# Performance work log

Hardware: AMD Instinct MI355X
Metric: run time of the kernel (lower is better)

## Reference

```python
import jax, jax.numpy as jnp
import numpy as np

VOCAB = 400001  # vocab_size + 1
H = 100         # n_hidden
B = 512
T = 25
FC = 128
NC = 2
FORGET_BIAS = 1.0


def setup_inputs() -> dict:
    key = jax.random.key(0)
    ks = jax.random.split(key, 8)
    features = jax.random.randint(ks[0], (B, T), 0, VOCAB, dtype=jnp.int32)
    embedding = jax.random.normal(ks[1], (VOCAB, H), dtype=jnp.float32) * 0.05
    # BasicLSTMCell kernel: [input_dim + hidden, 4*hidden], gate order (i, j, f, o)
    k1 = jax.random.normal(ks[2], (2 * H, 4 * H), dtype=jnp.float32) * 0.05
    b1 = jnp.zeros((4 * H,), dtype=jnp.float32)
    k2 = jax.random.normal(ks[3], (2 * H, 4 * H), dtype=jnp.float32) * 0.05
    b2 = jnp.zeros((4 * H,), dtype=jnp.float32)
    w_fc1 = jax.random.normal(ks[4], (H, FC), dtype=jnp.float32) * 0.05
    b_fc1 = jnp.zeros((FC,), dtype=jnp.float32)
    w_fc2 = jax.random.normal(ks[5], (FC, NC), dtype=jnp.float32) * 0.05
    b_fc2 = jnp.zeros((NC,), dtype=jnp.float32)
    return {"features": features, "embedding": embedding,
            "k1": k1, "b1": b1, "k2": k2, "b2": b2,
            "w_fc1": w_fc1, "b_fc1": b_fc1, "w_fc2": w_fc2, "b_fc2": b_fc2}


def _lstm_cell(c, h, x, kernel, bias):
    z = jnp.concatenate([x, h], axis=-1) @ kernel + bias  # [B, 4H]
    i, j, f, o = jnp.split(z, 4, axis=-1)
    c_new = c * jax.nn.sigmoid(f + FORGET_BIAS) + jax.nn.sigmoid(i) * jnp.tanh(j)
    h_new = jnp.tanh(c_new) * jax.nn.sigmoid(o)
    return c_new, h_new


def reference(features, embedding, k1, b1, k2, b2, w_fc1, b_fc1, w_fc2, b_fc2):
    x = embedding[features]                      # [B, T, H]
    xs = jnp.swapaxes(x, 0, 1)                   # [T, B, H] for scan over time
    batch = features.shape[0]
    zeros = jnp.zeros((batch, H), dtype=embedding.dtype)

    def step(carry, xt):
        c1, h1, c2, h2 = carry
        c1, h1 = _lstm_cell(c1, h1, xt, k1, b1)
        c2, h2 = _lstm_cell(c2, h2, h1, k2, b2)
        return (c1, h1, c2, h2), None

    (c1, h1, c2, h2), _ = jax.lax.scan(step, (zeros, zeros, zeros, zeros), xs)
    # dynamic_rnn outputs[:, -1, :] == final top-layer hidden state h2
    fc1 = h2 @ w_fc1 + b_fc1                     # linear, no activation (tf.layers.dense default)
    pred = fc1 @ w_fc2 + b_fc2                   # [B, num_classes] logits
    return pred
```

## Files before the change

### kernel.cpp

```cpp
#include <hip/hip_runtime.h>
#include <cstdint>
#include <cstddef>

#define VOCABSZ 400001
#define Hn 100
#define Tn 25
#define Bn 512
#define FCn 128
#define Rr 2
#define NBLK (Bn / Rr)
#define NTHR 512

typedef _Float16 half2_t __attribute__((ext_vector_type(2)));

__device__ __forceinline__ half2_t h2bits(unsigned v) {
    union { unsigned u; half2_t h; } x; x.u = v; return x.h;
}
__device__ __forceinline__ float fdot2f(half2_t a, half2_t b, float c) {
    return __builtin_amdgcn_fdot2(a, b, c, false);
}
__device__ __forceinline__ float sigm(float x) {
    return __fdividef(1.0f, 1.0f + __expf(-x));
}
__device__ __forceinline__ float tanh_fast(float x) {
    float e = __expf(2.0f * x);
    return __fdividef(e - 1.0f, e + 1.0f);
}

__global__ void prep_weights(const float* __restrict__ k1,
                             const float* __restrict__ k2,
                             uint4* __restrict__ WP) {
    int t = blockIdx.x * blockDim.x + threadIdx.x;
    if (t >= 2 * 25 * 400) return;
    int l   = t / 10000;
    int rem = t % 10000;
    int kq  = rem / 400;
    int o   = rem % 400;
    int u = o >> 2, g = o & 3;
    int c = g * 100 + u;
    const float* K = l ? k2 : k1;
    union { unsigned u32; half2_t h; } d[4];
    #pragma unroll
    for (int j = 0; j < 4; j++) {
        int k0 = 8 * kq + 2 * j;
        d[j].h.x = (_Float16)K[(k0    ) * 400 + c];
        d[j].h.y = (_Float16)K[(k0 + 1) * 400 + c];
    }
    uint4 v; v.x = d[0].u32; v.y = d[1].u32; v.z = d[2].u32; v.w = d[3].u32;
    WP[t] = v;
}

__device__ __forceinline__ float lstm_update(float z, int g, float& cst) {
    float t1 = __shfl_xor(z, 1);
    float t2 = __shfl_xor(z, 2);
    float t3 = __shfl_xor(t1, 2);
    bool g0 = (g & 1) != 0, g1 = (g & 2) != 0;
    float vi = g1 ? (g0 ? t3 : t2) : (g0 ? t1 : z);
    float vj = g1 ? (g0 ? t2 : t3) : (g0 ? z  : t1);
    float vf = g1 ? (g0 ? t1 : z ) : (g0 ? t3 : t2);
    float vo = g1 ? (g0 ? z  : t1) : (g0 ? t2 : t3);
    cst = cst * sigm(vf + 1.0f) + sigm(vi) * tanh_fast(vj);
    return tanh_fast(cst) * sigm(vo);
}

#define GEMV_LAYER(SRC0, SRC1, LIDX, BIAS, Z0, Z1)                           \
  {                                                                          \
    const uint4* _p0 = (const uint4*)(SRC0);                                 \
    const uint4* _p1 = (const uint4*)(SRC1);                                 \
    uint4 _vx = _p0[lane < 25 ? lane : 0];                                   \
    uint4 _vy = _p1[lane < 25 ? lane : 0];                                   \
    float _a0=0.f,_a1=0.f,_a2=0.f,_a3=0.f;                                   \
    float _d0=0.f,_d1=0.f,_d2=0.f,_d3=0.f;                                   \
    _Pragma("unroll")                                                        \
    for (int kq = 0; kq < 25; kq++) {                                        \
      uint4 _w = w[LIDX][kq];                                                \
      unsigned _s0 = (unsigned)__builtin_amdgcn_readlane((int)_vx.x, kq);    \
      unsigned _s1 = (unsigned)__builtin_amdgcn_readlane((int)_vx.y, kq);    \
      unsigned _s2 = (unsigned)__builtin_amdgcn_readlane((int)_vx.z, kq);    \
      unsigned _s3 = (unsigned)__builtin_amdgcn_readlane((int)_vx.w, kq);    \
      _a0 = fdot2f(h2bits(_w.x), h2bits(_s0), _a0);                          \
      _a1 = fdot2f(h2bits(_w.y), h2bits(_s1), _a1);                          \
      _a2 = fdot2f(h2bits(_w.z), h2bits(_s2), _a2);                          \
      _a3 = fdot2f(h2bits(_w.w), h2bits(_s3), _a3);                          \
      unsigned _t0 = (unsigned)__builtin_amdgcn_readlane((int)_vy.x, kq);    \
      unsigned _t1 = (unsigned)__builtin_amdgcn_readlane((int)_vy.y, kq);    \
      unsigned _t2 = (unsigned)__builtin_amdgcn_readlane((int)_vy.z, kq);    \
      unsigned _t3 = (unsigned)__builtin_amdgcn_readlane((int)_vy.w, kq);    \
      _d0 = fdot2f(h2bits(_w.x), h2bits(_t0), _d0);                          \
      _d1 = fdot2f(h2bits(_w.y), h2bits(_t1), _d1);                          \
      _d2 = fdot2f(h2bits(_w.z), h2bits(_t2), _d2);                          \
      _d3 = fdot2f(h2bits(_w.w), h2bits(_t3), _d3);                          \
    }                                                                        \
    Z0 = _a0 + _a1 + _a2 + _a3 + (BIAS);                                     \
    Z1 = _d0 + _d1 + _d2 + _d3 + (BIAS);                                     \
  }

__global__ __launch_bounds__(NTHR, 2) void lstm_main(
    const int*   __restrict__ features,
    const float* __restrict__ embedding,
    const float* __restrict__ b1,
    const float* __restrict__ b2,
    const float* __restrict__ w_fc1,
    const float* __restrict__ b_fc1,
    const float* __restrict__ w_fc2,
    const float* __restrict__ b_fc2,
    const uint4* __restrict__ WP,
    float*       __restrict__ out)
{
    __shared__ _Float16 xh1[Rr][200];
    __shared__ _Float16 xh2[Rr][200];
    __shared__ float    wred[8][2];

    const int tid  = threadIdx.x;
    const int lane = tid & 63;
    const int o    = (tid < 400) ? tid : 399;
    const int u = o >> 2, g = o & 3;
    const int c = g * 100 + u;
    const bool owner = (tid < 400);

    uint4 w[2][25];
    #pragma unroll
    for (int l = 0; l < 2; l++)
        #pragma unroll
        for (int kq = 0; kq < 25; kq++)
            w[l][kq] = WP[(l * 25 + kq) * 400 + o];

    const float bias1 = b1[c];
    const float bias2 = b2[c];

    if (tid < 200) {
        int r = tid / 100, uu = tid % 100;
        xh1[r][100 + uu] = (_Float16)0.0f;
        xh2[r][uu]       = (_Float16)0.0f;
        xh2[r][100 + uu] = (_Float16)0.0f;
    }
    if (tid < 100) {
        int r = tid / 50, p = tid % 50;
        int f0 = features[(blockIdx.x * Rr + r) * Tn + 0];
        float2 e = *(const float2*)(embedding + (size_t)f0 * Hn + 2 * p);
        half2_t h; h.x = (_Float16)e.x; h.y = (_Float16)e.y;
        ((half2_t*)&xh1[r][0])[p] = h;
    }
    __syncthreads();

    float c1[Rr] = {0.f, 0.f}, c2[Rr] = {0.f, 0.f};
    float h1v[Rr] = {0.f, 0.f}, h2v[Rr] = {0.f, 0.f};

    for (int step = 0; step < Tn; step++) {
        float2 epre = {0.f, 0.f};
        int prow = 0, pp = 0;
        if (tid < 448) {
            if (owner && g == 1 && step + 1 < Tn) {
                prow = (u >= 50);
                pp   = u % 50;
                int f1 = features[(blockIdx.x * Rr + prow) * Tn + step + 1];
                epre = *(const float2*)(embedding + (size_t)f1 * Hn + 2 * pp);
            }
            float z0, z1;
            GEMV_LAYER(&xh1[0][0], &xh1[1][0], 0, bias1, z0, z1);
            h1v[0] = lstm_update(z0, g, c1[0]);
            h1v[1] = lstm_update(z1, g, c1[1]);
        }
        __syncthreads();
        if (owner) {
            if (g == 0) {
                xh1[0][100 + u] = (_Float16)h1v[0];
                xh1[1][100 + u] = (_Float16)h1v[1];
                xh2[0][u]       = (_Float16)h1v[0];
                xh2[1][u]       = (_Float16)h1v[1];
            }
            if (g == 1 && step + 1 < Tn) {
                half2_t h; h.x = (_Float16)epre.x; h.y = (_Float16)epre.y;
                ((half2_t*)&xh1[prow][0])[pp] = h;
            }
        }
        __syncthreads();
        if (tid < 448) {
            float z0, z1;
            GEMV_LAYER(&xh2[0][0], &xh2[1][0], 1, bias2, z0, z1);
            h2v[0] = lstm_update(z0, g, c2[0]);
            h2v[1] = lstm_update(z1, g, c2[1]);
        }
        __syncthreads();
        if (owner && g == 0) {
            xh2[0][100 + u] = (_Float16)h2v[0];
            xh2[1][100 + u] = (_Float16)h2v[1];
        }
    }
    __syncthreads();

    if (tid < Rr * FCn) {
        int r = tid >> 7;
        int j = tid & 127;
        float acc = b_fc1[j];
        #pragma unroll 10
        for (int uu = 0; uu < Hn; uu++)
            acc = fmaf((float)xh2[r][100 + uu], w_fc1[uu * FCn + j], acc);
        float p0 = acc * w_fc2[2 * j + 0];
        float p1 = acc * w_fc2[2 * j + 1];
        #pragma unroll
        for (int off = 32; off > 0; off >>= 1) {
            p0 += __shfl_down(p0, off, 64);
            p1 += __shfl_down(p1, off, 64);
        }
        if (lane == 0) {
            int wv = tid >> 6;
            wred[wv][0] = p0;
            wred[wv][1] = p1;
        }
    }
    __syncthreads();
    if (tid < 4) {
        int r = tid >> 1, cls = tid & 1;
        out[(blockIdx.x * Rr + r) * 2 + cls] =
            wred[2 * r][cls] + wred[2 * r + 1][cls] + b_fc2[cls];
    }
}

extern "C" void kernel_launch(void* const* d_in, const int* in_sizes, int n_in,
                              void* d_out, int out_size, void* d_ws, size_t ws_size,
                              hipStream_t stream) {
    const int*   features  = (const int*)  d_in[0];
    const float* embedding = (const float*)d_in[1];
    const float* k1        = (const float*)d_in[2];
    const float* b1        = (const float*)d_in[3];
    const float* k2        = (const float*)d_in[4];
    const float* b2        = (const float*)d_in[5];
    const float* w_fc1     = (const float*)d_in[6];
    const float* b_fc1     = (const float*)d_in[7];
    const float* w_fc2     = (const float*)d_in[8];
    const float* b_fc2     = (const float*)d_in[9];

    uint4* WP = (uint4*)d_ws;

    prep_weights<<<(20000 + 255) / 256, 256, 0, stream>>>(k1, k2, WP);
    lstm_main<<<NBLK, NTHR, 0, stream>>>(features, embedding, b1, b2,
                                         w_fc1, b_fc1, w_fc2, b_fc2,
                                         WP, (float*)d_out);
}
```

Baseline: 344.1 us.

## Stage layer-1 LSTM weights in LDS and tile the weight-prep transpose

The main kernel previously kept both layers' packed fp16 weights in registers (50 uint4 per thread). That register pressure likely caused spills under the launch bounds. Now the layer-1 weights (about 160 KB) are copied once into LDS per block and read from there each step, while only the layer-2 weights stay in registers. This adds per-step LDS read traffic and a large up-front LDS fill, and uses almost the whole LDS, limiting the CU to one block. The prep kernel also now stages an 8x400 slab through shared memory so the global reads are coalesced.

```diff
diff --git a/kernel.cpp b/kernel.cpp
--- a/kernel.cpp
+++ b/kernel.cpp
@@ -27,27 +27,31 @@
     return __fdividef(e - 1.0f, e + 1.0f);
 }
 
-__global__ void prep_weights(const float* __restrict__ k1,
-                             const float* __restrict__ k2,
-                             uint4* __restrict__ WP) {
-    int t = blockIdx.x * blockDim.x + threadIdx.x;
-    if (t >= 2 * 25 * 400) return;
-    int l   = t / 10000;
-    int rem = t % 10000;
-    int kq  = rem / 400;
-    int o   = rem % 400;
-    int u = o >> 2, g = o & 3;
-    int c = g * 100 + u;
+__global__ __launch_bounds__(512) void prep_weights(const float* __restrict__ k1,
+                                                    const float* __restrict__ k2,
+                                                    uint4* __restrict__ WP) {
+    __shared__ float tile[8][400];
+    int l  = blockIdx.x / 25;
+    int kq = blockIdx.x % 25;
     const float* K = l ? k2 : k1;
-    union { unsigned u32; half2_t h; } d[4];
-    #pragma unroll
-    for (int j = 0; j < 4; j++) {
-        int k0 = 8 * kq + 2 * j;
-        d[j].h.x = (_Float16)K[(k0    ) * 400 + c];
-        d[j].h.y = (_Float16)K[(k0 + 1) * 400 + c];
-    }
-    uint4 v; v.x = d[0].u32; v.y = d[1].u32; v.z = d[2].u32; v.w = d[3].u32;
-    WP[t] = v;
+    for (int i = threadIdx.x; i < 8 * 400; i += 512) {
+        int row = i / 400, col = i % 400;
+        tile[row][col] = K[(8 * kq + row) * 400 + col];
+    }
+    __syncthreads();
+    int o = threadIdx.x;
+    if (o < 400) {
+        int u = o >> 2, g = o & 3;
+        int c = g * 100 + u;
+        union { unsigned u32; half2_t h; } d[4];
+        #pragma unroll
+        for (int j = 0; j < 4; j++) {
+            d[j].h.x = (_Float16)tile[2 * j][c];
+            d[j].h.y = (_Float16)tile[2 * j + 1][c];
+        }
+        uint4 v; v.x = d[0].u32; v.y = d[1].u32; v.z = d[2].u32; v.w = d[3].u32;
+        WP[(l * 25 + kq) * 400 + o] = v;
+    }
 }
 
 __device__ __forceinline__ float lstm_update(float z, int g, float& cst) {
@@ -63,7 +67,7 @@
     return tanh_fast(cst) * sigm(vo);
 }
 
-#define GEMV_LAYER(SRC0, SRC1, LIDX, BIAS, Z0, Z1)                           \
+#define GEMV_W(WGET, SRC0, SRC1, BIAS, Z0, Z1)                               \
   {                                                                          \
     const uint4* _p0 = (const uint4*)(SRC0);                                 \
     const uint4* _p1 = (const uint4*)(SRC1);                                 \
@@ -73,7 +77,7 @@
     float _d0=0.f,_d1=0.f,_d2=0.f,_d3=0.f;                                   \
     _Pragma("unroll")                                                        \
     for (int kq = 0; kq < 25; kq++) {                                        \
-      uint4 _w = w[LIDX][kq];                                                \
+      uint4 _w = (WGET);                                                     \
       unsigned _s0 = (unsigned)__builtin_amdgcn_readlane((int)_vx.x, kq);    \
       unsigned _s1 = (unsigned)__builtin_amdgcn_readlane((int)_vx.y, kq);    \
       unsigned _s2 = (unsigned)__builtin_amdgcn_readlane((int)_vx.z, kq);    \
@@ -107,8 +111,9 @@
     const uint4* __restrict__ WP,
     float*       __restrict__ out)
 {
-    __shared__ _Float16 xh1[Rr][200];
-    __shared__ _Float16 xh2[Rr][200];
+    __shared__ uint4    ldsK1[10000];
+    __shared__ alignas(16) _Float16 xh1[Rr][200];
+    __shared__ alignas(16) _Float16 xh2[Rr][200];
     __shared__ float    wred[8][2];
 
     const int tid  = threadIdx.x;
@@ -118,12 +123,12 @@
     const int c = g * 100 + u;
     const bool owner = (tid < 400);
 
-    uint4 w[2][25];
+    for (int i = tid; i < 10000; i += NTHR) ldsK1[i] = WP[i];
+
+    uint4 w2[25];
     #pragma unroll
-    for (int l = 0; l < 2; l++)
-        #pragma unroll
-        for (int kq = 0; kq < 25; kq++)
-            w[l][kq] = WP[(l * 25 + kq) * 400 + o];
+    for (int kq = 0; kq < 25; kq++)
+        w2[kq] = WP[(25 + kq) * 400 + o];
 
     const float bias1 = b1[c];
     const float bias2 = b2[c];
@@ -157,7 +162,7 @@
                 epre = *(const float2*)(embedding + (size_t)f1 * Hn + 2 * pp);
             }
             float z0, z1;
-            GEMV_LAYER(&xh1[0][0], &xh1[1][0], 0, bias1, z0, z1);
+            GEMV_W(ldsK1[kq * 400 + o], &xh1[0][0], &xh1[1][0], bias1, z0, z1);
             h1v[0] = lstm_update(z0, g, c1[0]);
             h1v[1] = lstm_update(z1, g, c1[1]);
         }
@@ -177,7 +182,7 @@
         __syncthreads();
         if (tid < 448) {
             float z0, z1;
-            GEMV_LAYER(&xh2[0][0], &xh2[1][0], 1, bias2, z0, z1);
+            GEMV_W(w2[kq], &xh2[0][0], &xh2[1][0], bias2, z0, z1);
             h2v[0] = lstm_update(z0, g, c2[0]);
             h2v[1] = lstm_update(z1, g, c2[1]);
         }
@@ -233,7 +238,7 @@
 
     uint4* WP = (uint4*)d_ws;
 
-    prep_weights<<<(20000 + 255) / 256, 256, 0, stream>>>(k1, k2, WP);
+    prep_weights<<<50, 512, 0, stream>>>(k1, k2, WP);
     lstm_main<<<NBLK, NTHR, 0, stream>>>(features, embedding, b1, b2,
                                          w_fc1, b_fc1, w_fc2, b_fc2,
                                          WP, (float*)d_out);
```

Measured after the change: 349.1 us. Within noise of the previous version (+1.5%).
